# Kernel tuning notes

Hardware: AMD Instinct MI355X
Metric: run time of the kernel (lower is better)

## Reference

```python
import jax, jax.numpy as jnp
import numpy as np

TAU = 16.0
R_L2 = 1e-4
N_CLASSES = 2
K_HIGH = 15   # up to 15 high-attention feats per bag
K_LOW = 5     # up to 5 low-attention feats per bag (every other, [::2])


def setup_inputs() -> dict:
    key = jax.random.key(0)
    ks = jax.random.split(key, 6)
    B, N, D = 16, 2048, 1024
    return {
        "fea": jax.random.normal(ks[0], (B, N, D), jnp.float32),
        "score": jax.random.uniform(ks[1], (B, N), jnp.float32),
        "label": jax.random.randint(ks[2], (B,), 0, N_CLASSES),
        "t_logit": jax.random.normal(ks[3], (1,), jnp.float32),
        "ori_logits": jax.random.normal(ks[4], (B, N_CLASSES), jnp.float32),
        "l2_wei": jax.random.uniform(ks[5], (1,), jnp.float32),
    }


def _take_first_k(sorted_fea, sel_mask, K):
    # gather the (at most K) True positions of sel_mask, in sorted order, into a
    # fixed [K, D] buffer with a validity mask (jit-friendly padding).
    order = jnp.argsort(~sel_mask)          # stable sort: selected positions first
    idx = order[:K]
    valid = jnp.arange(K) < sel_mask.sum()
    feats = jnp.where(valid[:, None], sorted_fea[idx], 0.0)
    return feats, valid


def _select_bag(feab, scoreb, gmax, gmin):
    order = jnp.argsort(scoreb)             # ascending, as torch.argsort
    sf = feab[order]                        # [N, D]
    ss = scoreb[order]                      # [N]
    # high-attention: score in [gmax-0.3, gmax], first 15 in sorted order
    hm = (ss >= gmax - 0.3) & (ss <= gmax)
    hrank = jnp.cumsum(hm) - 1
    H, mh = _take_first_k(sf, hm & (hrank < K_HIGH), K_HIGH)
    # low-attention: score in [gmin, gmin+1e-9], take [::2][:5]
    lm = (ss >= gmin) & (ss <= gmin + 1e-9)
    lrank = jnp.cumsum(lm) - 1
    lsel = lm & (lrank % 2 == 0) & ((lrank // 2) < K_LOW)
    L, ml = _take_first_k(sf, lsel, K_LOW)
    return H, mh, L, ml


def reference(fea, score, label, t_logit, ori_logits, l2_wei):
    B, _, D = fea.shape
    gmax = jnp.max(score)
    gmin = jnp.min(score)

    # per-bag sort + masked selection (the feature_dict update, starting empty)
    H, mh, L, ml = jax.vmap(_select_bag, in_axes=(0, 0, None, None))(fea, score, gmax, gmin)
    # H: [B,15,D] mh: [B,15]   L: [B,5,D] ml: [B,5]

    # memory bank = all selected features this batch (no truncation at these sizes)
    bank = jnp.concatenate([H.reshape(-1, D), L.reshape(-1, D)], axis=0)        # [B*20, D]
    bank_valid = jnp.concatenate([mh.reshape(-1), ml.reshape(-1)], axis=0)      # [B*20]
    bank_lab = jnp.concatenate(
        [jnp.repeat(label, K_HIGH), jnp.full((B * K_LOW,), N_CLASSES, label.dtype)])

    # queries: each bag's selected high feats target class label[b]; low feats target
    # the negative bucket (key == class_num)
    Q = jnp.concatenate([H, L], axis=1)                                          # [B,20,D]
    qv = jnp.concatenate([mh, ml], axis=1)                                       # [B,20]
    qt = jnp.concatenate(
        [jnp.broadcast_to(label[:, None], (B, K_HIGH)),
         jnp.full((B, K_LOW), N_CLASSES, label.dtype)], axis=1)                  # [B,20]

    E = jnp.exp(jnp.einsum('bkd,nd->bkn', Q, bank) / TAU) * bank_valid           # [B,20,B*20]
    den = E.sum(-1)
    num = jnp.where(bank_lab[None, None, :] == qt[:, :, None], E, 0.0).sum(-1)
    per = jnp.where(qv,
                    -jnp.log(jnp.where(qv, num, 1.0) / jnp.where(qv, den, 1.0)),
                    0.0)
    contrastive = jnp.mean(per.sum(-1) / qv.sum(-1))

    # adaptive cross entropy: -log(exp(t_logit) / sum(exp(ori_logits[i]))) averaged
    ce = jnp.mean(-jnp.log(jnp.exp(t_logit[0]) / jnp.sum(jnp.exp(ori_logits), axis=1)))
    Dm = jnp.mean(score) / jnp.max(score)
    l2 = R_L2 * (1.0 - Dm) ** 2 * l2_wei[0]
    return contrastive + ce + l2
```

## Files before the change

kernel.cpp:

```cpp
#include <hip/hip_runtime.h>
#include <math.h>

#define BB 16
#define NN 2048
#define DD 1024
#define KH 15
#define KL 5
#define NH 240
#define NBANK 320

#define WS_BAGMAX 0
#define WS_BAGMIN 16
#define WS_BAGSUM 32
#define WS_SELH   64
#define WS_SELL   320
#define WS_PNUM   512
#define WS_PDEN   1280

__global__ void k_stats(const float* __restrict__ score, float* __restrict__ ws) {
    int b = blockIdx.x, t = threadIdx.x;
    const float* sc = score + b * NN;
    float mx = -1e30f, mn = 1e30f, sm = 0.f;
    for (int j = t; j < NN; j += 256) {
        float s = sc[j];
        mx = fmaxf(mx, s); mn = fminf(mn, s); sm += s;
    }
    __shared__ float rmx[256], rmn[256], rsm[256];
    rmx[t] = mx; rmn[t] = mn; rsm[t] = sm;
    __syncthreads();
    for (int s2 = 128; s2 > 0; s2 >>= 1) {
        if (t < s2) {
            rmx[t] = fmaxf(rmx[t], rmx[t + s2]);
            rmn[t] = fminf(rmn[t], rmn[t + s2]);
            rsm[t] += rsm[t + s2];
        }
        __syncthreads();
    }
    if (t == 0) {
        ws[WS_BAGMAX + b] = rmx[0];
        ws[WS_BAGMIN + b] = rmn[0];
        ws[WS_BAGSUM + b] = rsm[0];
    }
}

__global__ void __launch_bounds__(256) k_select(const float* __restrict__ score,
                                                const float* __restrict__ ws,
                                                int* __restrict__ selH,
                                                int* __restrict__ selL) {
    int b = blockIdx.x, t = threadIdx.x;
    __shared__ float sgmax, sgmin;
    __shared__ unsigned long long list[NN];
    __shared__ int cnt;
    if (t == 0) {
        float mx = -1e30f, mn = 1e30f;
        for (int i = 0; i < BB; ++i) {
            mx = fmaxf(mx, ws[WS_BAGMAX + i]);
            mn = fminf(mn, ws[WS_BAGMIN + i]);
        }
        sgmax = mx; sgmin = mn; cnt = 0;
    }
    __syncthreads();
    const float* sc = score + b * NN;
    unsigned long long key[8];
    float sv[8];
    bool inb[8];
    int rk[8];
    #pragma unroll
    for (int j = 0; j < 8; ++j) {
        int i = t + 256 * j;
        float s = sc[i];
        sv[j] = s;
        key[j] = ((unsigned long long)__float_as_uint(s) << 32) | (unsigned)i;
    }

    float hlo = sgmax - 0.3f;
    #pragma unroll
    for (int j = 0; j < 8; ++j) {
        inb[j] = (sv[j] >= hlo);
        rk[j] = 0;
        if (inb[j]) { int p = atomicAdd(&cnt, 1); list[p] = key[j]; }
    }
    __syncthreads();
    int m = cnt;
    for (int j = 0; j < m; ++j) {
        unsigned long long lk = list[j];
        #pragma unroll
        for (int c = 0; c < 8; ++c) rk[c] += (inb[c] && (lk < key[c])) ? 1 : 0;
    }
    #pragma unroll
    for (int c = 0; c < 8; ++c)
        if (inb[c] && rk[c] < KH) selH[b * KH + rk[c]] = (int)(key[c] & 0xffffffffu);
    __syncthreads();
    if (t == 0) {
        int v = min(m, KH);
        for (int k = v; k < KH; ++k) selH[b * KH + k] = -1;
        cnt = 0;
    }
    __syncthreads();

    float llo = sgmin, lhi = sgmin + 1e-9f;
    #pragma unroll
    for (int j = 0; j < 8; ++j) {
        inb[j] = (sv[j] >= llo && sv[j] <= lhi);
        rk[j] = 0;
        if (inb[j]) { int p = atomicAdd(&cnt, 1); list[p] = key[j]; }
    }
    __syncthreads();
    m = cnt;
    for (int j = 0; j < m; ++j) {
        unsigned long long lk = list[j];
        #pragma unroll
        for (int c = 0; c < 8; ++c) rk[c] += (inb[c] && (lk < key[c])) ? 1 : 0;
    }
    #pragma unroll
    for (int c = 0; c < 8; ++c) {
        if (inb[c]) {
            int r = rk[c];
            if ((r & 1) == 0 && (r >> 1) < KL)
                selL[b * KL + (r >> 1)] = (int)(key[c] & 0xffffffffu);
        }
    }
    if (t == 0) {
        int v = min((m + 1) / 2, KL);
        for (int k = v; k < KL; ++k) selL[b * KL + k] = -1;
    }
}

__global__ void __launch_bounds__(256) k_gram(const float* __restrict__ fea,
                                              const int* __restrict__ selH,
                                              const int* __restrict__ selL,
                                              const int* __restrict__ label,
                                              float* __restrict__ ws) {
    int blk = blockIdx.x, t = threadIdx.x;
    int g = blk >> 1, h = blk & 1;
    int q0 = g * 4;
    __shared__ int s_row[NBANK], s_lab[NBANK];
    __shared__ int s_qrow[4], s_qt[4];
    for (int n = t; n < NBANK; n += 256) {
        int bn, in_, ln;
        if (n < NH) { bn = n / KH; in_ = selH[n]; ln = label[bn]; }
        else        { bn = (n - NH) / KL; in_ = selL[n - NH]; ln = 2; }
        s_row[n] = (in_ >= 0) ? bn * NN + in_ : -1;
        s_lab[n] = ln;
    }
    if (t < 4) {
        int q = q0 + t; int bq, iq, qt;
        if (q < NH) { bq = q / KH; iq = selH[q]; qt = label[bq]; }
        else        { bq = (q - NH) / KL; iq = selL[q - NH]; qt = 2; }
        s_qrow[t] = (iq >= 0) ? bq * NN + iq : 0;
        s_qt[t] = qt;
    }
    __syncthreads();
    int w = t >> 6, l = t & 63;
    const float4* qp0 = (const float4*)(fea + (size_t)s_qrow[0] * DD);
    const float4* qp1 = (const float4*)(fea + (size_t)s_qrow[1] * DD);
    const float4* qp2 = (const float4*)(fea + (size_t)s_qrow[2] * DD);
    const float4* qp3 = (const float4*)(fea + (size_t)s_qrow[3] * DD);
    int qt0 = s_qt[0], qt1 = s_qt[1], qt2 = s_qt[2], qt3 = s_qt[3];
    float d0 = 0, d1 = 0, d2 = 0, d3 = 0;
    float n0 = 0, n1 = 0, n2 = 0, n3 = 0;
    for (int k = 0; k < 40; ++k) {
        int n = h * 160 + w * 40 + k;
        int rn = s_row[n];
        if (rn < 0) continue;
        const float4* np_ = (const float4*)(fea + (size_t)rn * DD);
        float a0 = 0, a1 = 0, a2 = 0, a3 = 0;
        #pragma unroll
        for (int c = 0; c < 4; ++c) {
            float4 nv = np_[c * 64 + l];
            float4 v;
            v = qp0[c * 64 + l]; a0 += nv.x * v.x + nv.y * v.y + nv.z * v.z + nv.w * v.w;
            v = qp1[c * 64 + l]; a1 += nv.x * v.x + nv.y * v.y + nv.z * v.z + nv.w * v.w;
            v = qp2[c * 64 + l]; a2 += nv.x * v.x + nv.y * v.y + nv.z * v.z + nv.w * v.w;
            v = qp3[c * 64 + l]; a3 += nv.x * v.x + nv.y * v.y + nv.z * v.z + nv.w * v.w;
        }
        #pragma unroll
        for (int s2 = 32; s2 > 0; s2 >>= 1) {
            a0 += __shfl_xor(a0, s2);
            a1 += __shfl_xor(a1, s2);
            a2 += __shfl_xor(a2, s2);
            a3 += __shfl_xor(a3, s2);
        }
        int ln = s_lab[n];
        float e;
        e = __expf(a0 * 0.0625f); d0 += e; if (ln == qt0) n0 += e;
        e = __expf(a1 * 0.0625f); d1 += e; if (ln == qt1) n1 += e;
        e = __expf(a2 * 0.0625f); d2 += e; if (ln == qt2) n2 += e;
        e = __expf(a3 * 0.0625f); d3 += e; if (ln == qt3) n3 += e;
    }
    __shared__ float s_pn[4][4], s_pd[4][4];
    if (l == 0) {
        s_pn[w][0] = n0; s_pn[w][1] = n1; s_pn[w][2] = n2; s_pn[w][3] = n3;
        s_pd[w][0] = d0; s_pd[w][1] = d1; s_pd[w][2] = d2; s_pd[w][3] = d3;
    }
    __syncthreads();
    if (t < 4) {
        float num = 0, den = 0;
        for (int ww = 0; ww < 4; ++ww) { num += s_pn[ww][t]; den += s_pd[ww][t]; }
        ws[WS_PNUM + (q0 + t) * 2 + h] = num;
        ws[WS_PDEN + (q0 + t) * 2 + h] = den;
    }
}

__global__ void __launch_bounds__(320) k_final(const float* __restrict__ ws,
                                               const int* __restrict__ selH,
                                               const int* __restrict__ selL,
                                               const float* __restrict__ t_logit,
                                               const float* __restrict__ ori,
                                               const float* __restrict__ l2w,
                                               float* __restrict__ out) {
    int t = threadIdx.x;
    __shared__ float sper[NBANK], sval[NBANK];
    __shared__ float sc16[16], sce[16];
    if (t < NBANK) {
        float num = ws[WS_PNUM + 2 * t] + ws[WS_PNUM + 2 * t + 1];
        float den = ws[WS_PDEN + 2 * t] + ws[WS_PDEN + 2 * t + 1];
        bool valid = (t < NH) ? (selH[t] >= 0) : (selL[t - NH] >= 0);
        sper[t] = valid ? (logf(den) - logf(num)) : 0.f;
        sval[t] = valid ? 1.f : 0.f;
    }
    __syncthreads();
    if (t < 16) {
        float s = 0, c = 0;
        for (int k = 0; k < KH; ++k) { s += sper[t * KH + k]; c += sval[t * KH + k]; }
        for (int k = 0; k < KL; ++k) { int q = NH + t * KL + k; s += sper[q]; c += sval[q]; }
        sc16[t] = s / c;
    } else if (t >= 64 && t < 80) {
        int b = t - 64;
        sce[b] = logf(expf(ori[2 * b]) + expf(ori[2 * b + 1])) - t_logit[0];
    }
    __syncthreads();
    if (t == 0) {
        float contrast = 0, ce = 0;
        for (int b = 0; b < 16; ++b) { contrast += sc16[b]; ce += sce[b]; }
        contrast *= (1.f / 16.f); ce *= (1.f / 16.f);
        float gmax = -1e30f, ssum = 0.f;
        for (int i = 0; i < 16; ++i) {
            gmax = fmaxf(gmax, ws[WS_BAGMAX + i]);
            ssum += ws[WS_BAGSUM + i];
        }
        float Dm = (ssum / (float)(BB * NN)) / gmax;
        float l2 = 1e-4f * (1.f - Dm) * (1.f - Dm) * l2w[0];
        out[0] = contrast + ce + l2;
    }
}

extern "C" void kernel_launch(void* const* d_in, const int* in_sizes, int n_in,
                              void* d_out, int out_size, void* d_ws, size_t ws_size,
                              hipStream_t stream) {
    const float* fea     = (const float*)d_in[0];
    const float* score   = (const float*)d_in[1];
    const int*   label   = (const int*)d_in[2];
    const float* t_logit = (const float*)d_in[3];
    const float* ori     = (const float*)d_in[4];
    const float* l2_wei  = (const float*)d_in[5];
    float* ws  = (float*)d_ws;
    int* selH  = (int*)d_ws + WS_SELH;
    int* selL  = (int*)d_ws + WS_SELL;
    float* out = (float*)d_out;

    hipLaunchKernelGGL(k_stats,  dim3(BB),  dim3(256), 0, stream, score, ws);
    hipLaunchKernelGGL(k_select, dim3(BB),  dim3(256), 0, stream, score, ws, selH, selL);
    hipLaunchKernelGGL(k_gram,   dim3(160), dim3(256), 0, stream, fea, selH, selL, label, ws);
    hipLaunchKernelGGL(k_final,  dim3(1),   dim3(320), 0, stream, ws, selH, selL, t_logit, ori, l2_wei, out);
}
```

Before: 262.1 us.

## Replace rank-count selection with iterative argmin, split gram wider, fuse final reduction

The selection kernel replaces the shared-list plus all-pairs rank counting with repeated block-wide argmin passes: up to 15 rounds for high-attention features and 10 rounds for low-attention ones, each using wave shuffles and two barriers. This removes the O(m) loop over candidates, which can be long when many scores fall within 0.3 of the max. The gram kernel now splits each query group over 4 bank slices instead of 2 (320 blocks), and the last block to finish, found through an atomic counter with threadfences, does the final reduction. That fusion removes the separate k_final launch. In exchange it adds atomic-counter synchronisation and more partial sums to combine.

New measurement: 232.3 us, median of 2. 1.13x faster.

```diff
diff --git a/kernel.cpp b/kernel.cpp
--- a/kernel.cpp
+++ b/kernel.cpp
@@ -12,13 +12,15 @@
 #define WS_BAGMAX 0
 #define WS_BAGMIN 16
 #define WS_BAGSUM 32
+#define WS_DONE   48
 #define WS_SELH   64
 #define WS_SELL   320
 #define WS_PNUM   512
-#define WS_PDEN   1280
+#define WS_PDEN   1792
 
 __global__ void k_stats(const float* __restrict__ score, float* __restrict__ ws) {
     int b = blockIdx.x, t = threadIdx.x;
+    if (b == 0 && t == 0) ((int*)ws)[WS_DONE] = 0;
     const float* sc = score + b * NN;
     float mx = -1e30f, mn = 1e30f, sm = 0.f;
     for (int j = t; j < NN; j += 256) {
@@ -47,24 +49,24 @@
                                                 const float* __restrict__ ws,
                                                 int* __restrict__ selH,
                                                 int* __restrict__ selL) {
+    const unsigned long long INV = ~0ULL;
     int b = blockIdx.x, t = threadIdx.x;
+    int w = t >> 6, l = t & 63;
     __shared__ float sgmax, sgmin;
-    __shared__ unsigned long long list[NN];
-    __shared__ int cnt;
+    __shared__ unsigned long long wmin[4];
     if (t == 0) {
         float mx = -1e30f, mn = 1e30f;
         for (int i = 0; i < BB; ++i) {
             mx = fmaxf(mx, ws[WS_BAGMAX + i]);
             mn = fminf(mn, ws[WS_BAGMIN + i]);
         }
-        sgmax = mx; sgmin = mn; cnt = 0;
+        sgmax = mx; sgmin = mn;
     }
     __syncthreads();
     const float* sc = score + b * NN;
     unsigned long long key[8];
     float sv[8];
-    bool inb[8];
-    int rk[8];
+    bool alive[8];
     #pragma unroll
     for (int j = 0; j < 8; ++j) {
         int i = t + 256 * j;
@@ -75,64 +77,71 @@
 
     float hlo = sgmax - 0.3f;
     #pragma unroll
-    for (int j = 0; j < 8; ++j) {
-        inb[j] = (sv[j] >= hlo);
-        rk[j] = 0;
-        if (inb[j]) { int p = atomicAdd(&cnt, 1); list[p] = key[j]; }
-    }
-    __syncthreads();
-    int m = cnt;
-    for (int j = 0; j < m; ++j) {
-        unsigned long long lk = list[j];
-        #pragma unroll
-        for (int c = 0; c < 8; ++c) rk[c] += (inb[c] && (lk < key[c])) ? 1 : 0;
-    }
-    #pragma unroll
-    for (int c = 0; c < 8; ++c)
-        if (inb[c] && rk[c] < KH) selH[b * KH + rk[c]] = (int)(key[c] & 0xffffffffu);
-    __syncthreads();
-    if (t == 0) {
-        int v = min(m, KH);
-        for (int k = v; k < KH; ++k) selH[b * KH + k] = -1;
-        cnt = 0;
-    }
-    __syncthreads();
+    for (int j = 0; j < 8; ++j) alive[j] = (sv[j] >= hlo);
+    int r = 0;
+    for (; r < KH; ++r) {
+        unsigned long long v = INV;
+        #pragma unroll
+        for (int j = 0; j < 8; ++j) if (alive[j] && key[j] < v) v = key[j];
+        #pragma unroll
+        for (int s2 = 32; s2 > 0; s2 >>= 1) {
+            unsigned long long o = __shfl_xor(v, s2);
+            if (o < v) v = o;
+        }
+        if (l == 0) wmin[w] = v;
+        __syncthreads();
+        unsigned long long win = wmin[0];
+        #pragma unroll
+        for (int ww = 1; ww < 4; ++ww) if (wmin[ww] < win) win = wmin[ww];
+        __syncthreads();
+        if (win == INV) break;
+        if (t == 0) selH[b * KH + r] = (int)(win & 0xffffffffu);
+        #pragma unroll
+        for (int j = 0; j < 8; ++j) alive[j] = alive[j] && (key[j] != win);
+    }
+    if (t == 0) for (int k = r; k < KH; ++k) selH[b * KH + k] = -1;
 
     float llo = sgmin, lhi = sgmin + 1e-9f;
     #pragma unroll
-    for (int j = 0; j < 8; ++j) {
-        inb[j] = (sv[j] >= llo && sv[j] <= lhi);
-        rk[j] = 0;
-        if (inb[j]) { int p = atomicAdd(&cnt, 1); list[p] = key[j]; }
-    }
-    __syncthreads();
-    m = cnt;
-    for (int j = 0; j < m; ++j) {
-        unsigned long long lk = list[j];
-        #pragma unroll
-        for (int c = 0; c < 8; ++c) rk[c] += (inb[c] && (lk < key[c])) ? 1 : 0;
-    }
-    #pragma unroll
-    for (int c = 0; c < 8; ++c) {
-        if (inb[c]) {
-            int r = rk[c];
-            if ((r & 1) == 0 && (r >> 1) < KL)
-                selL[b * KL + (r >> 1)] = (int)(key[c] & 0xffffffffu);
-        }
-    }
-    if (t == 0) {
-        int v = min((m + 1) / 2, KL);
-        for (int k = v; k < KL; ++k) selL[b * KL + k] = -1;
-    }
+    for (int j = 0; j < 8; ++j) alive[j] = (sv[j] >= llo && sv[j] <= lhi);
+    int nsel = 0;
+    for (int rr = 0; rr < 2 * KL; ++rr) {
+        unsigned long long v = INV;
+        #pragma unroll
+        for (int j = 0; j < 8; ++j) if (alive[j] && key[j] < v) v = key[j];
+        #pragma unroll
+        for (int s2 = 32; s2 > 0; s2 >>= 1) {
+            unsigned long long o = __shfl_xor(v, s2);
+            if (o < v) v = o;
+        }
+        if (l == 0) wmin[w] = v;
+        __syncthreads();
+        unsigned long long win = wmin[0];
+        #pragma unroll
+        for (int ww = 1; ww < 4; ++ww) if (wmin[ww] < win) win = wmin[ww];
+        __syncthreads();
+        if (win == INV) break;
+        if ((rr & 1) == 0) {
+            if (t == 0) selL[b * KL + (rr >> 1)] = (int)(win & 0xffffffffu);
+            nsel++;
+        }
+        #pragma unroll
+        for (int j = 0; j < 8; ++j) alive[j] = alive[j] && (key[j] != win);
+    }
+    if (t == 0) for (int k = nsel; k < KL; ++k) selL[b * KL + k] = -1;
 }
 
 __global__ void __launch_bounds__(256) k_gram(const float* __restrict__ fea,
                                               const int* __restrict__ selH,
                                               const int* __restrict__ selL,
                                               const int* __restrict__ label,
-                                              float* __restrict__ ws) {
+                                              const float* __restrict__ t_logit,
+                                              const float* __restrict__ ori,
+                                              const float* __restrict__ l2w,
+                                              float* __restrict__ ws,
+                                              float* __restrict__ out) {
     int blk = blockIdx.x, t = threadIdx.x;
-    int g = blk >> 1, h = blk & 1;
+    int g = blk >> 2, h = blk & 3;
     int q0 = g * 4;
     __shared__ int s_row[NBANK], s_lab[NBANK];
     __shared__ int s_qrow[4], s_qt[4];
@@ -159,8 +168,8 @@
     int qt0 = s_qt[0], qt1 = s_qt[1], qt2 = s_qt[2], qt3 = s_qt[3];
     float d0 = 0, d1 = 0, d2 = 0, d3 = 0;
     float n0 = 0, n1 = 0, n2 = 0, n3 = 0;
-    for (int k = 0; k < 40; ++k) {
-        int n = h * 160 + w * 40 + k;
+    for (int k = 0; k < 20; ++k) {
+        int n = h * 80 + w * 20 + k;
         int rn = s_row[n];
         if (rn < 0) continue;
         const float4* np_ = (const float4*)(fea + (size_t)rn * DD);
@@ -197,27 +206,29 @@
     if (t < 4) {
         float num = 0, den = 0;
         for (int ww = 0; ww < 4; ++ww) { num += s_pn[ww][t]; den += s_pd[ww][t]; }
-        ws[WS_PNUM + (q0 + t) * 2 + h] = num;
-        ws[WS_PDEN + (q0 + t) * 2 + h] = den;
-    }
-}
-
-__global__ void __launch_bounds__(320) k_final(const float* __restrict__ ws,
-                                               const int* __restrict__ selH,
-                                               const int* __restrict__ selL,
-                                               const float* __restrict__ t_logit,
-                                               const float* __restrict__ ori,
-                                               const float* __restrict__ l2w,
-                                               float* __restrict__ out) {
-    int t = threadIdx.x;
+        ws[WS_PNUM + (q0 + t) * 4 + h] = num;
+        ws[WS_PDEN + (q0 + t) * 4 + h] = den;
+    }
+
+    __shared__ int s_old;
+    __threadfence();
+    if (t == 0) s_old = atomicAdd((int*)ws + WS_DONE, 1);
+    __syncthreads();
+    if (s_old != 320 - 1) return;
+    __threadfence();
+
     __shared__ float sper[NBANK], sval[NBANK];
     __shared__ float sc16[16], sce[16];
-    if (t < NBANK) {
-        float num = ws[WS_PNUM + 2 * t] + ws[WS_PNUM + 2 * t + 1];
-        float den = ws[WS_PDEN + 2 * t] + ws[WS_PDEN + 2 * t + 1];
-        bool valid = (t < NH) ? (selH[t] >= 0) : (selL[t - NH] >= 0);
-        sper[t] = valid ? (logf(den) - logf(num)) : 0.f;
-        sval[t] = valid ? 1.f : 0.f;
+    for (int q = t; q < NBANK; q += 256) {
+        float num = 0, den = 0;
+        #pragma unroll
+        for (int hh = 0; hh < 4; ++hh) {
+            num += ws[WS_PNUM + q * 4 + hh];
+            den += ws[WS_PDEN + q * 4 + hh];
+        }
+        bool valid = (q < NH) ? (selH[q] >= 0) : (selL[q - NH] >= 0);
+        sper[q] = valid ? (logf(den) - logf(num)) : 0.f;
+        sval[q] = valid ? 1.f : 0.f;
     }
     __syncthreads();
     if (t < 16) {
@@ -261,6 +272,6 @@
 
     hipLaunchKernelGGL(k_stats,  dim3(BB),  dim3(256), 0, stream, score, ws);
     hipLaunchKernelGGL(k_select, dim3(BB),  dim3(256), 0, stream, score, ws, selH, selL);
-    hipLaunchKernelGGL(k_gram,   dim3(160), dim3(256), 0, stream, fea, selH, selL, label, ws);
-    hipLaunchKernelGGL(k_final,  dim3(1),   dim3(320), 0, stream, ws, selH, selL, t_logit, ori, l2_wei, out);
-}
+    hipLaunchKernelGGL(k_gram,   dim3(320), dim3(256), 0, stream, fea, selH, selL, label,
+                       t_logit, ori, l2_wei, ws, out);
+}
```
